# Performance work log

Hardware: AMD Instinct MI355X
Metric: run time of the kernel (lower is better)

The kernel has to match this reference:

```python
import jax, jax.numpy as jnp
import numpy as np

B, NQ, NM, NHR, D, H, FF = 16, 100, 5440, 4096, 256, 8, 2048

def _ln(x, w, b):
    m = x.mean(-1, keepdims=True)
    v = ((x - m) ** 2).mean(-1, keepdims=True)
    return (x - m) * jax.lax.rsqrt(v + 1e-5) * w + b

def setup_inputs():
    key = jax.random.key(0)
    ks = iter(jax.random.split(key, 32))
    def rn(shape, s=1.0):
        return jax.random.normal(next(ks), shape, jnp.float32) * s
    return {
        'tgt': rn((B, NQ, D)),
        'memory': rn((B, NM, D)),
        'memory_hr': rn((B, NHR, D)),
        'prior_attn_bias': rn((B, NQ, NM)),
        'query_pos': rn((B, NQ, D)),
        'ln_cross_w': jnp.ones((D,)), 'ln_cross_b': jnp.zeros((D,)),
        'q_w': rn((D, D), 0.02), 'q_b': jnp.zeros((D,)),
        'k_w': rn((D, D), 0.02), 'k_b': jnp.zeros((D,)),
        'v_w': rn((D, D), 0.02), 'v_b': jnp.zeros((D,)),
        'out_w': rn((D, D), 0.02), 'out_b': jnp.zeros((D,)),
        'ln_self_w': jnp.ones((D,)), 'ln_self_b': jnp.zeros((D,)),
        'sa_in_w': rn((3 * D, D), 0.02), 'sa_in_b': jnp.zeros((3 * D,)),
        'sa_out_w': rn((D, D), 0.02), 'sa_out_b': jnp.zeros((D,)),
        'ln_ffn_w': jnp.ones((D,)), 'ln_ffn_b': jnp.zeros((D,)),
        'lin1_w': rn((FF, D), 0.02), 'lin1_b': jnp.zeros((FF,)),
        'lin2_w': rn((D, FF), 0.02), 'lin2_b': jnp.zeros((D,)),
        'me_w': rn((D, D), 0.02), 'me_b': jnp.zeros((D,)),
    }

def reference(tgt, memory, memory_hr, prior_attn_bias, query_pos,
              ln_cross_w, ln_cross_b, q_w, q_b, k_w, k_b, v_w, v_b,
              out_w, out_b, ln_self_w, ln_self_b, sa_in_w, sa_in_b,
              sa_out_w, sa_out_b, ln_ffn_w, ln_ffn_b, lin1_w, lin1_b,
              lin2_w, lin2_b, me_w, me_b):
    b, nq, d = tgt.shape
    nm = memory.shape[1]
    h = H
    dh = d // h
    scale = dh ** -0.5
    # ---- cross-attention with additive prior bias (eval mode: dropout = id) ----
    x = _ln(tgt, ln_cross_w, ln_cross_b)
    q = ((x + query_pos) @ q_w.T + q_b).reshape(b, nq, h, dh)
    k = (memory @ k_w.T + k_b).reshape(b, nm, h, dh)
    v = (memory @ v_w.T + v_b).reshape(b, nm, h, dh)
    attn = jnp.einsum('bqhd,bmhd->bhqm', q, k) * scale + prior_attn_bias[:, None]  # [b,h,nq,nm]
    a = jax.nn.softmax(attn, axis=-1)
    o = jnp.einsum('bhqm,bmhd->bqhd', a, v).reshape(b, nq, d)
    tgt = tgt + (o @ out_w.T + out_b)
    # ---- self-attention (torch nn.MultiheadAttention, batch_first, eval) ----
    z = _ln(tgt, ln_self_w, ln_self_b)
    zq = z + query_pos
    qs = (zq @ sa_in_w[:d].T + sa_in_b[:d]).reshape(b, nq, h, dh)
    ks = (zq @ sa_in_w[d:2 * d].T + sa_in_b[d:2 * d]).reshape(b, nq, h, dh)
    vs = (z @ sa_in_w[2 * d:].T + sa_in_b[2 * d:]).reshape(b, nq, h, dh)
    sattn = jax.nn.softmax(jnp.einsum('bqhd,bmhd->bhqm', qs, ks) * scale, axis=-1)
    so = jnp.einsum('bhqm,bmhd->bqhd', sattn, vs).reshape(b, nq, d)
    tgt = tgt + (so @ sa_out_w.T + sa_out_b)
    # ---- FFN ----
    y = _ln(tgt, ln_ffn_w, ln_ffn_b)
    y = jax.nn.gelu(y @ lin1_w.T + lin1_b, approximate=False) @ lin2_w.T + lin2_b
    tgt = tgt + y
    # ---- mask branch ----
    mask_logits = jnp.einsum('bqd,bmd->bqm', tgt @ me_w.T + me_b, memory_hr)
    return (tgt, mask_logits)
```

## Files before the change

### kernel.cpp

```cpp
#include <hip/hip_runtime.h>

typedef unsigned short u16;
typedef unsigned int u32;
typedef __bf16 bf16x8 __attribute__((ext_vector_type(8)));
typedef float f32x4 __attribute__((ext_vector_type(4)));

#define NCH 34

__device__ __forceinline__ u16 f2b(float f) {
  u32 u = __float_as_uint(f);
  u32 r = (u + 0x7fffu + ((u >> 16) & 1u)) >> 16;
  return (u16)r;
}
__device__ __forceinline__ float b2f(u16 h) {
  return __uint_as_float(((u32)h) << 16);
}
__device__ __forceinline__ bf16x8 zero8() {
  union { uint4 u; bf16x8 v; } z; z.u = make_uint4(0u, 0u, 0u, 0u); return z.v;
}
__device__ __forceinline__ u32 cvtpk(float lo, float hi) {
  u32 r;
  asm("v_cvt_pk_bf16_f32 %0, %1, %2" : "=v"(r) : "v"(lo), "v"(hi));
  return r;
}

struct Seg { const float* in; u16* out; int n4; };
struct PrepArgs {
  Seg seg[7];
  const float *k_w, *v_w, *k_b, *v_b, *pbias;
  u16 *Wf, *biasT;
  float *kvB;
};

__global__ __launch_bounds__(256)
void prep_kernel(PrepArgs a)
{
  __shared__ float S[100][69];
  const int bx = blockIdx.x, tid = threadIdx.x;
  if (bx < 1472) {
    int bxr = bx;
#pragma unroll
    for (int k = 0; k < 7; ++k) {
      const int nb = a.seg[k].n4 >> 8;
      if (bxr < nb) {
        const int i = bxr * 256 + tid;
        const float4 f = *(const float4*)(a.seg[k].in + (size_t)i * 4);
        uint2 pk; pk.x = cvtpk(f.x, f.y); pk.y = cvtpk(f.z, f.w);
        *(uint2*)(a.seg[k].out + (size_t)i * 4) = pk;
        return;
      }
      bxr -= nb;
    }
    return;
  } else if (bx < 1536) {
    const int i = bx - 1472, gI = i >> 3, ks = i & 7;
    const int nt = tid >> 6, lane = tid & 63, lr = lane & 15, g = lane >> 4;
    const float* src = (gI < 4 ? a.k_w + (size_t)(gI * 64 + nt * 16 + lr) * 256
                               : a.v_w + (size_t)((gI - 4) * 64 + nt * 16 + lr) * 256)
                       + ks * 32 + g * 8;
    const float4 f0 = *(const float4*)src;
    const float4 f1 = *(const float4*)(src + 4);
    uint4 pk;
    pk.x = cvtpk(f0.x, f0.y); pk.y = cvtpk(f0.z, f0.w);
    pk.z = cvtpk(f1.x, f1.y); pk.w = cvtpk(f1.z, f1.w);
    *(uint4*)(a.Wf + (size_t)((gI * 8 + ks) * 4 + nt) * 512 + lane * 8) = pk;
  } else if (bx < 1538) {
    const int i = (bx - 1536) * 256 + tid;
    a.kvB[i] = (i < 256) ? a.k_b[i] : a.v_b[i - 256];
  } else {
    const int bt = bx - 1538;
    const int b = bt / 85, m0 = (bt - b * 85) * 64;
    for (int idx = tid; idx < 1600; idx += 256) {
      const int q = idx >> 4, seg = idx & 15;
      const float4 v = *(const float4*)(a.pbias + (size_t)(b * 100 + q) * 5440 + m0 + seg * 4);
      S[q][seg * 4 + 0] = v.x; S[q][seg * 4 + 1] = v.y;
      S[q][seg * 4 + 2] = v.z; S[q][seg * 4 + 3] = v.w;
    }
    __syncthreads();
    for (int idx = tid; idx < 1792; idx += 256) {
      const int m = idx / 28, qg = (idx % 28) * 4;
      u16 h[4];
#pragma unroll
      for (int r = 0; r < 4; ++r) {
        const int q = qg + r;
        h[r] = (q < 100) ? f2b(S[q][m]) : (u16)0;
      }
      uint2 pk;
      pk.x = (u32)h[0] | ((u32)h[1] << 16);
      pk.y = (u32)h[2] | ((u32)h[3] << 16);
      *(uint2*)(a.biasT + ((size_t)(b * 5440 + m0 + m)) * 112 + qg) = pk;
    }
  }
}

template<int ROWS>
__device__ __forceinline__ void ln_stage(const float* __restrict__ x, int row0,
    const float* __restrict__ w, const float* __restrict__ b,
    const float* __restrict__ pos, u16* As)
{
  const int tid = threadIdx.x, lane = tid & 63, wid = tid >> 6;
  const float4 wv = *(const float4*)(w + lane * 4);
  const float4 bv = *(const float4*)(b + lane * 4);
#pragma unroll
  for (int rr = 0; rr < ROWS / 4; ++rr) {
    const int rl = wid * (ROWS / 4) + rr;
    const size_t o = (size_t)(row0 + rl) * 256 + lane * 4;
    const float4 v = *(const float4*)(x + o);
    float s = v.x + v.y + v.z + v.w;
#pragma unroll
    for (int m = 1; m < 64; m <<= 1) s += __shfl_xor(s, m);
    const float mean = s * (1.f / 256.f);
    const float d0 = v.x - mean, d1 = v.y - mean, d2 = v.z - mean, d3 = v.w - mean;
    float ss = d0 * d0 + d1 * d1 + d2 * d2 + d3 * d3;
#pragma unroll
    for (int m = 1; m < 64; m <<= 1) ss += __shfl_xor(ss, m);
    const float rs = rsqrtf(ss * (1.f / 256.f) + 1e-5f);
    float y0 = d0 * rs * wv.x + bv.x;
    float y1 = d1 * rs * wv.y + bv.y;
    float y2 = d2 * rs * wv.z + bv.z;
    float y3 = d3 * rs * wv.w + bv.w;
    if (pos) {
      const float4 pv = *(const float4*)(pos + o);
      y0 += pv.x; y1 += pv.y; y2 += pv.z; y3 += pv.w;
    }
    uint2 pk; pk.x = cvtpk(y0, y1); pk.y = cvtpk(y2, y3);
    const int byte = (rl * 512 + lane * 8) ^ ((rl & 7) << 4);
    *(uint2*)((char*)As + byte) = pk;
  }
}

__device__ __forceinline__ void gemm16x128(const u16* As, const u16* __restrict__ W,
                                           u16 (*Ws)[40], f32x4 acc[2])
{
  const int tid = threadIdx.x, lane = tid & 63, wid = tid >> 6;
  const int g = lane >> 4, lr = lane & 15;
  for (int k0 = 0; k0 < 256; k0 += 32) {
    for (int cid = tid; cid < 512; cid += 256) {
      const int r = cid >> 2, cg = (cid & 3) * 8;
      *(uint4*)&Ws[r][cg] = *(const uint4*)(W + (size_t)r * 256 + k0 + cg);
    }
    __syncthreads();
    const int abyte = (lr * 512 + k0 * 2 + g * 16) ^ ((lr & 7) << 4);
    const bf16x8 af = *(const bf16x8*)((const char*)As + abyte);
#pragma unroll
    for (int nt = 0; nt < 2; ++nt) {
      const bf16x8 bfr = *(const bf16x8*)&Ws[wid * 32 + nt * 16 + lr][g * 8];
      acc[nt] = __builtin_amdgcn_mfma_f32_16x16x32_bf16(af, bfr, acc[nt], 0, 0, 0);
    }
    __syncthreads();
  }
}

__global__ __launch_bounds__(256)
void qproj_kernel(const float* __restrict__ x, const float* __restrict__ lnw,
                  const float* __restrict__ lnb, const float* __restrict__ pos,
                  const u16* __restrict__ W, const float* __restrict__ bias,
                  u16* __restrict__ out, float scale)
{
  __shared__ u16 As[16 * 256];
  __shared__ u16 Ws[128][40];
  const int tid = threadIdx.x, lane = tid & 63, wid = tid >> 6;
  const int g = lane >> 4, lr = lane & 15;
  const int row0 = blockIdx.x * 16, n0 = blockIdx.y * 128;
  ln_stage<16>(x, row0, lnw, lnb, pos, As);
  f32x4 acc[2] = {};
  gemm16x128(As, W + (size_t)n0 * 256, Ws, acc);
#pragma unroll
  for (int nt = 0; nt < 2; ++nt) {
    const int col = n0 + wid * 32 + nt * 16 + lr;
    const float bv = bias[col];
#pragma unroll
    for (int r = 0; r < 4; ++r) {
      const int row = row0 + g * 4 + r;
      out[(size_t)row * 256 + col] = f2b((acc[nt][r] + bv) * scale);
    }
  }
}

__global__ __launch_bounds__(256)
void sain_kernel(const float* __restrict__ x, const float* __restrict__ lnw,
                 const float* __restrict__ lnb, const float* __restrict__ pos,
                 const u16* __restrict__ W, const float* __restrict__ bias,
                 float* __restrict__ qkb, float* __restrict__ vsb)
{
  __shared__ u16 As[16 * 256];
  __shared__ u16 Ws[128][40];
  const int tid = threadIdx.x, lane = tid & 63, wid = tid >> 6;
  const int g = lane >> 4, lr = lane & 15;
  const int row0 = blockIdx.x * 16, y = blockIdx.y;
  ln_stage<16>(x, row0, lnw, lnb, (y < 4) ? pos : nullptr, As);
  f32x4 acc[2] = {};
  gemm16x128(As, W + (size_t)y * 128 * 256, Ws, acc);
#pragma unroll
  for (int nt = 0; nt < 2; ++nt) {
    const int cl = wid * 32 + nt * 16 + lr;
    const float bv = bias[y * 128 + cl];
#pragma unroll
    for (int r = 0; r < 4; ++r) {
      const int row = row0 + g * 4 + r;
      const float v = acc[nt][r] + bv;
      if (y < 4) qkb[(size_t)row * 512 + y * 128 + cl] = v;
      else       vsb[(size_t)row * 256 + (y - 4) * 128 + cl] = v;
    }
  }
}

__global__ __launch_bounds__(256)
void ffn1_kernel(const float* __restrict__ x, const float* __restrict__ lnw,
                 const float* __restrict__ lnb, const u16* __restrict__ W,
                 const float* __restrict__ bias, u16* __restrict__ out)
{
  __shared__ u16 As[64 * 256];
  __shared__ u16 Ws[256][40];
  const int tid = threadIdx.x, lane = tid & 63, wid = tid >> 6;
  const int g = lane >> 4, lr = lane & 15;
  const int row0 = blockIdx.x * 64, n0 = blockIdx.y * 256;
  ln_stage<64>(x, row0, lnw, lnb, nullptr, As);
  f32x4 acc[16] = {};
  for (int k0 = 0; k0 < 256; k0 += 32) {
    for (int cid = tid; cid < 1024; cid += 256) {
      const int r = cid >> 2, cg = (cid & 3) * 8;
      *(uint4*)&Ws[r][cg] = *(const uint4*)(W + (size_t)(n0 + r) * 256 + k0 + cg);
    }
    __syncthreads();
    const int arow = wid * 16 + lr;
    const int abyte = (arow * 512 + k0 * 2 + g * 16) ^ ((arow & 7) << 4);
    const bf16x8 af = *(const bf16x8*)((const char*)As + abyte);
#pragma unroll
    for (int nt = 0; nt < 16; ++nt) {
      const bf16x8 bfr = *(const bf16x8*)&Ws[nt * 16 + lr][g * 8];
      acc[nt] = __builtin_amdgcn_mfma_f32_16x16x32_bf16(af, bfr, acc[nt], 0, 0, 0);
    }
    __syncthreads();
  }
#pragma unroll
  for (int nt = 0; nt < 16; ++nt) {
    const int col = n0 + nt * 16 + lr;
    const float bv = bias[col];
#pragma unroll
    for (int r = 0; r < 4; ++r) {
      const int row = row0 + wid * 16 + g * 4 + r;
      float v = acc[nt][r] + bv;
      v = 0.5f * v * (1.f + erff(v * 0.70710678118654752f));
      out[(size_t)row * 2048 + col] = f2b(v);
    }
  }
}

template<int BM, int BN, int WM, int WN, int GELU_, int RES_, int OF32, int OBF>
__global__ __launch_bounds__(256)
void gemm_kernel(const u16* __restrict__ Ap, const u16* __restrict__ W,
                 const float* __restrict__ bias, const float* __restrict__ res,
                 float* __restrict__ Cf, u16* __restrict__ Cb,
                 int M, int N, int K, float scale)
{
  constexpr int WROWS = BM / WM;
  constexpr int WCOLS = BN / WN;
  constexpr int MT = WROWS / 16;
  constexpr int NT = WCOLS / 16;
  static_assert(WM * WN == 4, "4 waves");
  __shared__ u16 As[BM][40];
  __shared__ u16 Ws[BN][40];
  const int tid = threadIdx.x, lane = tid & 63, wid = tid >> 6;
  const int g = lane >> 4, lr = lane & 15;
  const int m0 = blockIdx.x * BM, n0 = blockIdx.y * BN;
  const int wm = wid / WN, wn = wid % WN;
  f32x4 acc[MT][NT] = {};
  for (int k0 = 0; k0 < K; k0 += 32) {
    for (int cid = tid; cid < BM * 4; cid += 256) {
      int r = cid >> 2, cg = (cid & 3) * 8;
      *(uint4*)&As[r][cg] = *(const uint4*)(Ap + (size_t)(m0 + r) * K + k0 + cg);
    }
    for (int cid = tid; cid < BN * 4; cid += 256) {
      int r = cid >> 2, cg = (cid & 3) * 8;
      *(uint4*)&Ws[r][cg] = *(const uint4*)(W + (size_t)(n0 + r) * K + k0 + cg);
    }
    __syncthreads();
    bf16x8 af[MT], bfr[NT];
#pragma unroll
    for (int mt = 0; mt < MT; ++mt) af[mt] = *(const bf16x8*)&As[wm * WROWS + mt * 16 + lr][g * 8];
#pragma unroll
    for (int nt = 0; nt < NT; ++nt) bfr[nt] = *(const bf16x8*)&Ws[wn * WCOLS + nt * 16 + lr][g * 8];
#pragma unroll
    for (int mt = 0; mt < MT; ++mt)
#pragma unroll
      for (int nt = 0; nt < NT; ++nt)
        acc[mt][nt] = __builtin_amdgcn_mfma_f32_16x16x32_bf16(af[mt], bfr[nt], acc[mt][nt], 0, 0, 0);
    __syncthreads();
  }
#pragma unroll
  for (int mt = 0; mt < MT; ++mt)
#pragma unroll
    for (int nt = 0; nt < NT; ++nt) {
      const int col = n0 + wn * WCOLS + nt * 16 + lr;
      const float bv = bias[col];
#pragma unroll
      for (int r = 0; r < 4; ++r) {
        const int row = m0 + wm * WROWS + mt * 16 + g * 4 + r;
        float v = (acc[mt][nt][r] + bv) * scale;
        if constexpr (GELU_) v = 0.5f * v * (1.f + erff(v * 0.70710678118654752f));
        if constexpr (RES_) v += res[(size_t)row * N + col];
        if constexpr (OF32) Cf[(size_t)row * N + col] = v;
        if constexpr (OBF) Cb[(size_t)row * N + col] = f2b(v);
      }
    }
}

__global__ __launch_bounds__(512, 4)
void kv_gemm_kernel(const float* __restrict__ A, const u16* __restrict__ Wf,
                    const float* __restrict__ biasKV,
                    u16* __restrict__ Kb, u16* __restrict__ Vt)
{
  __shared__ u16 As[64 * 256];
  __shared__ u16 Vs[256 * 64];
  const int tid = threadIdx.x, lane = tid & 63, wid = tid >> 6;
  const int g = lane >> 4, lr = lane & 15;
  const int bidx = blockIdx.x / 85, t = blockIdx.x - bidx * 85;
  const int row0 = blockIdx.x * 64;

  for (int ch = tid; ch < 2048; ch += 512) {
    const int r = ch >> 5, c8 = (ch & 31) * 8;
    const float* ap = A + (size_t)(row0 + r) * 256 + c8;
    const float4 f0 = *(const float4*)ap;
    const float4 f1 = *(const float4*)(ap + 4);
    uint4 pk;
    pk.x = cvtpk(f0.x, f0.y);
    pk.y = cvtpk(f0.z, f0.w);
    pk.z = cvtpk(f1.x, f1.y);
    pk.w = cvtpk(f1.z, f1.w);
    const int byte = r * 512 + c8 * 2;
    *(uint4*)((char*)As + (byte ^ ((r & 7) << 4))) = pk;
  }
  __syncthreads();

  const u16* wbase = Wf + (size_t)wid * 8 * 4 * 512 + lane * 8;
  f32x4 acc[4][4] = {};
#pragma unroll 2
  for (int ks = 0; ks < 8; ++ks) {
    bf16x8 bfv[4], af[4];
#pragma unroll
    for (int nt = 0; nt < 4; ++nt)
      bfv[nt] = *(const bf16x8*)(wbase + (ks * 4 + nt) * 512);
#pragma unroll
    for (int mt = 0; mt < 4; ++mt) {
      const int r = mt * 16 + lr;
      const int byte = r * 512 + ks * 64 + g * 16;
      af[mt] = *(const bf16x8*)((const char*)As + (byte ^ ((r & 7) << 4)));
    }
#pragma unroll
    for (int mt = 0; mt < 4; ++mt)
#pragma unroll
      for (int nt = 0; nt < 4; ++nt)
        acc[mt][nt] = __builtin_amdgcn_mfma_f32_16x16x32_bf16(af[mt], bfv[nt], acc[mt][nt], 0, 0, 0);
  }

  const int isV = wid >> 2;
  if (isV) {
#pragma unroll
    for (int nt = 0; nt < 4; ++nt) {
      const int col = (wid - 4) * 64 + nt * 16 + lr;
      const float bv = biasKV[256 + col];
#pragma unroll
      for (int a = 0; a < 2; ++a)
#pragma unroll
        for (int r = 0; r < 4; ++r) {
          const u32 val = cvtpk(acc[2 * a][nt][r] + bv, acc[2 * a + 1][nt][r] + bv);
          const int byte = (col * 128 + a * 64 + g * 16 + r * 4) ^ ((col & 7) << 4);
          *(u32*)((char*)Vs + byte) = val;
        }
    }
  }
  __syncthreads();

  if (!isV) {
#pragma unroll
    for (int nt = 0; nt < 4; ++nt) {
      const int col = wid * 64 + nt * 16 + lr;
      const float bv = biasKV[col];
#pragma unroll
      for (int mt = 0; mt < 4; ++mt)
#pragma unroll
        for (int r = 0; r < 4; r += 2) {
          const u32 pk = cvtpk(acc[mt][nt][r] + bv, acc[mt][nt][r + 1] + bv);
          const int rowA = mt * 16 + g * 4 + r;
          const int rowB = rowA + 1;
          *(u16*)((char*)As + ((rowA * 512 + col * 2) ^ ((rowA & 7) << 4))) = (u16)pk;
          *(u16*)((char*)As + ((rowB * 512 + col * 2) ^ ((rowB & 7) << 4))) = (u16)(pk >> 16);
        }
    }
  } else {
    const size_t vbase = (size_t)bidx * 256 * 5440 + (size_t)t * 64;
    const int t2 = tid - 256;
#pragma unroll
    for (int p = 0; p < 8; ++p) {
      const int idx = p * 256 + t2;
      const int col = idx >> 3, chunk = idx & 7;
      const int lbyte = col * 128 + ((chunk * 16) ^ ((col & 7) << 4));
      const uint4 v = *(const uint4*)((const char*)Vs + lbyte);
      *(uint4*)(Vt + vbase + (size_t)col * 5440 + chunk * 8) = v;
    }
  }
  __syncthreads();
#pragma unroll
  for (int p = 0; p < 4; ++p) {
    const int idx = p * 512 + tid;
    const int row = idx >> 5, c16 = idx & 31;
    const int lbyte = row * 512 + ((c16 * 16) ^ ((row & 7) << 4));
    const uint4 v = *(const uint4*)((const char*)As + lbyte);
    *(uint4*)(Kb + (size_t)(row0 + row) * 256 + c16 * 8) = v;
  }
}

__global__ __launch_bounds__(256, 3)
void cross_attn_kernel(const u16* __restrict__ Q, const u16* __restrict__ Kb,
                       const u16* __restrict__ Vt, const u16* __restrict__ biasT,
                       float* __restrict__ Opart, float* __restrict__ ML)
{
  __shared__ u32 P32[4][112][20];
  const int tid = threadIdx.x, lane = tid & 63, wid = tid >> 6;
  const int g = lane >> 4, lr = lane & 15;
  const int b = blockIdx.y, c = blockIdx.x;
  const int head = blockIdx.z * 4 + wid;
  const int m_base = c * (5440 / NCH);
  const f32x4 zf = {0.f, 0.f, 0.f, 0.f};

  bf16x8 qf[7];
#pragma unroll
  for (int mt = 0; mt < 7; ++mt) {
    int qr = mt * 16 + lr;
    qf[mt] = (qr < 100) ? *(const bf16x8*)&Q[(size_t)(b * 100 + qr) * 256 + head * 32 + g * 8]
                        : zero8();
  }
  float Mst[7];
  f32x4 Lp[7];
  f32x4 Oa[7][2];
#pragma unroll
  for (int mt = 0; mt < 7; ++mt) { Mst[mt] = -1e30f; Lp[mt] = zf; Oa[mt][0] = zf; Oa[mt][1] = zf; }

  for (int s = 0; s < (5440 / NCH) / 32; ++s) {
    const int m0 = m_base + s * 32;
    const bf16x8 kf0 = *(const bf16x8*)&Kb[(size_t)(b * 5440 + m0 + lr) * 256 + head * 32 + g * 8];
    const bf16x8 kf1 = *(const bf16x8*)&Kb[(size_t)(b * 5440 + m0 + 16 + lr) * 256 + head * 32 + g * 8];
    const size_t vrow = ((size_t)(b * 8 + head) * 32 + lr) * 5440 + m0 + g * 8;
    const bf16x8 vf0 = *(const bf16x8*)&Vt[vrow];
    const bf16x8 vf1 = *(const bf16x8*)&Vt[vrow + 16 * 5440];
    const u16* bb = biasT + ((size_t)(b * 5440 + m0 + lr)) * 112 + g * 4;
#pragma unroll
    for (int mt = 0; mt < 7; ++mt) {
      f32x4 s0 = __builtin_amdgcn_mfma_f32_16x16x32_bf16(qf[mt], kf0, zf, 0, 0, 0);
      f32x4 s1 = __builtin_amdgcn_mfma_f32_16x16x32_bf16(qf[mt], kf1, zf, 0, 0, 0);
      const uint2 b0 = *(const uint2*)(bb + mt * 16);
      const uint2 b1 = *(const uint2*)(bb + 16 * 112 + mt * 16);
      s0[0] += b2f((u16)b0.x);      s0[1] += b2f((u16)(b0.x >> 16));
      s0[2] += b2f((u16)b0.y);      s0[3] += b2f((u16)(b0.y >> 16));
      s1[0] += b2f((u16)b1.x);      s1[1] += b2f((u16)(b1.x >> 16));
      s1[2] += b2f((u16)b1.y);      s1[3] += b2f((u16)(b1.y >> 16));
      float mx = fmaxf(fmaxf(fmaxf(s0[0], s0[1]), fmaxf(s0[2], s0[3])),
                       fmaxf(fmaxf(s1[0], s1[1]), fmaxf(s1[2], s1[3])));
#pragma unroll
      for (int d = 1; d < 16; d <<= 1) mx = fmaxf(mx, __shfl_xor(mx, d, 16));
      const float newM = fmaxf(Mst[mt], mx);
      const float al = __expf(Mst[mt] - newM);
      Mst[mt] = newM;
      f32x4 p0, p1;
#pragma unroll
      for (int r = 0; r < 4; ++r) {
        p0[r] = __expf(s0[r] - newM);
        p1[r] = __expf(s1[r] - newM);
      }
      Lp[mt] = Lp[mt] * al + (p0 + p1);
      Oa[mt][0] *= al;
      Oa[mt][1] *= al;
#pragma unroll
      for (int r = 0; r < 4; ++r)
        P32[wid][mt * 16 + g * 4 + r][lr] = (u32)f2b(p0[r]) | ((u32)f2b(p1[r]) << 16);
    }
#pragma unroll
    for (int mt = 0; mt < 7; ++mt) {
      const bf16x8 pa = *(const bf16x8*)&P32[wid][mt * 16 + lr][g * 4];
      Oa[mt][0] = __builtin_amdgcn_mfma_f32_16x16x32_bf16(pa, vf0, Oa[mt][0], 0, 0, 0);
      Oa[mt][1] = __builtin_amdgcn_mfma_f32_16x16x32_bf16(pa, vf1, Oa[mt][1], 0, 0, 0);
    }
  }
  const int bh = b * 8 + head;
#pragma unroll
  for (int mt = 0; mt < 7; ++mt)
#pragma unroll
    for (int r = 0; r < 4; ++r) {
      const int qr = mt * 16 + g * 4 + r;
      if (qr < 100) {
        float L = Lp[mt][r];
#pragma unroll
        for (int d = 1; d < 16; d <<= 1) L += __shfl_xor(L, d, 16);
        const size_t rb = (size_t)(bh * NCH + c) * 100 + qr;
        Opart[rb * 32 + lr] = Oa[mt][0][r];
        Opart[rb * 32 + 16 + lr] = Oa[mt][1][r];
        if (lr == 0) { ML[rb * 2] = Mst[mt]; ML[rb * 2 + 1] = L; }
      }
    }
}

__global__ __launch_bounds__(256)
void reduce_attn_kernel(const float* __restrict__ Opart, const float* __restrict__ ML,
                        u16* __restrict__ outb)
{
  const int row = blockIdx.x;
  const int b = row / 100, q = row % 100;
  const int h = threadIdx.x >> 5, d = threadIdx.x & 31;
  const int bh = b * 8 + h;
  float gm = -1e30f;
  for (int c = 0; c < NCH; ++c) gm = fmaxf(gm, ML[((size_t)(bh * NCH + c) * 100 + q) * 2]);
  float l = 0.f, o = 0.f;
  for (int c = 0; c < NCH; ++c) {
    const size_t rb = (size_t)(bh * NCH + c) * 100 + q;
    const float w = __expf(ML[rb * 2] - gm);
    l += ML[rb * 2 + 1] * w;
    o += Opart[rb * 32 + d] * w;
  }
  outb[(size_t)row * 256 + h * 32 + d] = f2b(o / l);
}

__global__ __launch_bounds__(128)
void self_attn_kernel(const float* __restrict__ qk, const float* __restrict__ vs,
                      u16* __restrict__ so)
{
  __shared__ u16 kk[100][36];
  __shared__ u16 vv[100][36];
  __shared__ float S[100][101];
  const int b = blockIdx.x >> 3, h = blockIdx.x & 7;
  const int t = threadIdx.x;
  for (int e = t; e < 3200; e += 128) {
    const int r = e >> 5, cq = e & 31;
    kk[r][cq] = f2b(qk[(size_t)(b * 100 + r) * 512 + 256 + h * 32 + cq]);
    vv[r][cq] = f2b(vs[(size_t)(b * 100 + r) * 256 + h * 32 + cq]);
  }
  __syncthreads();
  if (t < 100) {
    float qr_[32];
#pragma unroll
    for (int cq = 0; cq < 32; ++cq) qr_[cq] = qk[(size_t)(b * 100 + t) * 512 + h * 32 + cq];
    for (int m = 0; m < 100; ++m) {
      float dp = 0.f;
#pragma unroll
      for (int cq = 0; cq < 32; ++cq) dp += qr_[cq] * b2f(kk[m][cq]);
      S[t][m] = dp * 0.17677669529663687f;
    }
    float mx = -1e30f;
    for (int m = 0; m < 100; ++m) mx = fmaxf(mx, S[t][m]);
    float sum = 0.f;
    for (int m = 0; m < 100; ++m) { const float p = __expf(S[t][m] - mx); S[t][m] = p; sum += p; }
    const float inv = 1.f / sum;
    float o[32];
#pragma unroll
    for (int cq = 0; cq < 32; ++cq) o[cq] = 0.f;
    for (int m = 0; m < 100; ++m) {
      const float p = S[t][m];
#pragma unroll
      for (int cq = 0; cq < 32; ++cq) o[cq] += p * b2f(vv[m][cq]);
    }
#pragma unroll
    for (int cq = 0; cq < 32; ++cq)
      so[(size_t)(b * 100 + t) * 256 + h * 32 + cq] = f2b(o[cq] * inv);
  }
}

__global__ __launch_bounds__(256)
void mask_gemm_kernel(const u16* __restrict__ tm, const float* __restrict__ hr,
                      float* __restrict__ out)
{
  __shared__ u16 As[112][40];
  __shared__ u16 Bs[64][40];
  const int tid = threadIdx.x, lane = tid & 63, wid = tid >> 6;
  const int g = lane >> 4, lr = lane & 15;
  const int b = blockIdx.y, n0 = blockIdx.x * 64;
  f32x4 acc[7] = {};
  for (int k0 = 0; k0 < 256; k0 += 32) {
    for (int cid = tid; cid < 448; cid += 256) {
      const int r = cid >> 2, cg = (cid & 3) * 8;
      uint4 val = {0u, 0u, 0u, 0u};
      if (r < 100) val = *(const uint4*)&tm[(size_t)(b * 100 + r) * 256 + k0 + cg];
      *(uint4*)&As[r][cg] = val;
    }
    {
      const int r = tid >> 2, cg = (tid & 3) * 8;
      const float* hp = hr + (size_t)(b * 4096 + n0 + r) * 256 + k0 + cg;
      float4 f0 = *(const float4*)hp;
      float4 f1 = *(const float4*)(hp + 4);
      uint4 pk;
      pk.x = cvtpk(f0.x, f0.y); pk.y = cvtpk(f0.z, f0.w);
      pk.z = cvtpk(f1.x, f1.y); pk.w = cvtpk(f1.z, f1.w);
      *(uint4*)&Bs[r][cg] = pk;
    }
    __syncthreads();
    const bf16x8 bfr = *(const bf16x8*)&Bs[wid * 16 + lr][g * 8];
#pragma unroll
    for (int mt = 0; mt < 7; ++mt) {
      const bf16x8 af = *(const bf16x8*)&As[mt * 16 + lr][g * 8];
      acc[mt] = __builtin_amdgcn_mfma_f32_16x16x32_bf16(af, bfr, acc[mt], 0, 0, 0);
    }
    __syncthreads();
  }
#pragma unroll
  for (int mt = 0; mt < 7; ++mt)
#pragma unroll
    for (int r = 0; r < 4; ++r) {
      const int qr = mt * 16 + g * 4 + r;
      if (qr < 100)
        out[(size_t)(b * 100 + qr) * 4096 + n0 + wid * 16 + lr] = acc[mt][r];
    }
}

extern "C" void kernel_launch(void* const* d_in, const int* in_sizes, int n_in,
                              void* d_out, int out_size, void* d_ws, size_t ws_size,
                              hipStream_t stream)
{
  (void)in_sizes; (void)n_in; (void)out_size; (void)ws_size;
  const float* tgt      = (const float*)d_in[0];
  const float* memory   = (const float*)d_in[1];
  const float* memhr    = (const float*)d_in[2];
  const float* pbias    = (const float*)d_in[3];
  const float* qpos     = (const float*)d_in[4];
  const float* lncw     = (const float*)d_in[5];
  const float* lncb     = (const float*)d_in[6];
  const float* q_w      = (const float*)d_in[7];
  const float* q_b      = (const float*)d_in[8];
  const float* k_w      = (const float*)d_in[9];
  const float* k_b      = (const float*)d_in[10];
  const float* v_w      = (const float*)d_in[11];
  const float* v_b      = (const float*)d_in[12];
  const float* out_w    = (const float*)d_in[13];
  const float* out_b    = (const float*)d_in[14];
  const float* lnsw     = (const float*)d_in[15];
  const float* lnsb     = (const float*)d_in[16];
  const float* sa_in_w  = (const float*)d_in[17];
  const float* sa_in_b  = (const float*)d_in[18];
  const float* sa_out_w = (const float*)d_in[19];
  const float* sa_out_b = (const float*)d_in[20];
  const float* lnfw     = (const float*)d_in[21];
  const float* lnfb     = (const float*)d_in[22];
  const float* l1w      = (const float*)d_in[23];
  const float* l1b      = (const float*)d_in[24];
  const float* l2w      = (const float*)d_in[25];
  const float* l2b      = (const float*)d_in[26];
  const float* me_w     = (const float*)d_in[27];
  const float* me_b     = (const float*)d_in[28];
  float* outf = (float*)d_out;

  char* ws = (char*)d_ws;
  size_t off = 0;
  auto alloc = [&](size_t bytes) -> void* {
    void* p = ws + off;
    off = (off + bytes + 255) & ~(size_t)255;
    return p;
  };
  u16*   Wf    = (u16*)alloc((size_t)131072 * 2);
  u16*   qW    = (u16*)alloc((size_t)65536 * 2);
  u16*   outW  = (u16*)alloc((size_t)65536 * 2);
  u16*   saW   = (u16*)alloc((size_t)196608 * 2);
  u16*   saoW  = (u16*)alloc((size_t)65536 * 2);
  u16*   l1W   = (u16*)alloc((size_t)524288 * 2);
  u16*   l2W   = (u16*)alloc((size_t)524288 * 2);
  u16*   meW   = (u16*)alloc((size_t)65536 * 2);
  float* kvB   = (float*)alloc((size_t)512 * 4);
  u16*   biasT = (u16*)alloc((size_t)9748480 * 2);
  u16*   Qb    = (u16*)alloc((size_t)409600 * 2);
  u16*   Kb    = (u16*)alloc((size_t)22282240 * 2);
  u16*   Vt    = (u16*)alloc((size_t)22282240 * 2);
  float* Opart = (float*)alloc((size_t)(128 * NCH * 100 * 32) * 4);
  float* MLp   = (float*)alloc((size_t)(128 * NCH * 100 * 2) * 4);
  u16*   attno = (u16*)alloc((size_t)409600 * 2);
  float* tgt1  = (float*)alloc((size_t)409600 * 4);
  float* qkb   = (float*)alloc((size_t)819200 * 4);
  float* vsb   = (float*)alloc((size_t)409600 * 4);
  u16*   sob   = (u16*)alloc((size_t)409600 * 2);
  float* tgt2  = (float*)alloc((size_t)409600 * 4);
  u16*   hb    = (u16*)alloc((size_t)3276800 * 2);
  u16*   t3b   = (u16*)alloc((size_t)409600 * 2);
  u16*   tmb   = (u16*)alloc((size_t)409600 * 2);

  const float SCALE = 0.17677669529663687f;

  PrepArgs pa;
  pa.seg[0] = {q_w,      qW,   16384};
  pa.seg[1] = {out_w,    outW, 16384};
  pa.seg[2] = {sa_in_w,  saW,  49152};
  pa.seg[3] = {sa_out_w, saoW, 16384};
  pa.seg[4] = {l1w,      l1W,  131072};
  pa.seg[5] = {l2w,      l2W,  131072};
  pa.seg[6] = {me_w,     meW,  16384};
  pa.k_w = k_w; pa.v_w = v_w; pa.k_b = k_b; pa.v_b = v_b; pa.pbias = pbias;
  pa.Wf = Wf; pa.biasT = biasT; pa.kvB = kvB;
  prep_kernel<<<2898, 256, 0, stream>>>(pa);

  qproj_kernel<<<dim3(100, 2), 256, 0, stream>>>(tgt, lncw, lncb, qpos, qW, q_b, Qb, SCALE);
  kv_gemm_kernel<<<dim3(1360), 512, 0, stream>>>(memory, Wf, kvB, Kb, Vt);
  cross_attn_kernel<<<dim3(NCH, 16, 2), 256, 0, stream>>>(Qb, Kb, Vt, biasT, Opart, MLp);
  reduce_attn_kernel<<<1600, 256, 0, stream>>>(Opart, MLp, attno);
  gemm_kernel<16, 128, 1, 4, 0, 1, 1, 0><<<dim3(100, 2), 256, 0, stream>>>(
      attno, outW, out_b, tgt, tgt1, nullptr, 1600, 256, 256, 1.f);

  sain_kernel<<<dim3(100, 6), 256, 0, stream>>>(tgt1, lnsw, lnsb, qpos, saW, sa_in_b, qkb, vsb);
  self_attn_kernel<<<128, 128, 0, stream>>>(qkb, vsb, sob);
  gemm_kernel<16, 128, 1, 4, 0, 1, 1, 0><<<dim3(100, 2), 256, 0, stream>>>(
      sob, saoW, sa_out_b, tgt1, tgt2, nullptr, 1600, 256, 256, 1.f);

  ffn1_kernel<<<dim3(25, 8), 256, 0, stream>>>(tgt2, lnfw, lnfb, l1W, l1b, hb);
  gemm_kernel<16, 128, 1, 4, 0, 1, 1, 1><<<dim3(100, 2), 256, 0, stream>>>(
      hb, l2W, l2b, tgt2, outf, t3b, 1600, 256, 2048, 1.f);

  gemm_kernel<16, 128, 1, 4, 0, 0, 0, 1><<<dim3(100, 2), 256, 0, stream>>>(
      t3b, meW, me_b, nullptr, nullptr, tmb, 1600, 256, 256, 1.f);
  mask_gemm_kernel<<<dim3(64, 16), 256, 0, stream>>>(tmb, memhr, outf + 409600);
}
```

Baseline: 343.4 us.

## Pre-swizzle attention bias into MFMA fragment layout and prefetch per step

The prep kernel now writes the prior bias in a layout that matches the MFMA accumulator fragments, so each lane loads one 16-byte vector per query tile instead of two scattered 8-byte loads. The cross-attention loop prefetches all seven bias vectors at the start of each key step. The change also adds s_setprio around the MFMA sections, replaces the manual bf16 packing with v_cvt_pk_bf16_f32, and raises the occupancy hint to 4. Holding the prefetched bias in registers and asking for higher occupancy may increase register pressure or cause spills, and the prep kernel now launches more, smaller blocks.

```diff
diff --git a/kernel.cpp b/kernel.cpp
--- a/kernel.cpp
+++ b/kernel.cpp
@@ -6,6 +6,7 @@
 typedef float f32x4 __attribute__((ext_vector_type(4)));
 
 #define NCH 34
+#define NSTEP 5
 
 __device__ __forceinline__ u16 f2b(float f) {
   u32 u = __float_as_uint(f);
@@ -28,14 +29,15 @@
 struct PrepArgs {
   Seg seg[7];
   const float *k_w, *v_w, *k_b, *v_b, *pbias;
-  u16 *Wf, *biasT;
+  u16 *Wf;
+  uint4 *biasT4;
   float *kvB;
 };
 
 __global__ __launch_bounds__(256)
 void prep_kernel(PrepArgs a)
 {
-  __shared__ float S[100][69];
+  __shared__ float S[100][34];
   const int bx = blockIdx.x, tid = threadIdx.x;
   if (bx < 1472) {
     int bxr = bx;
@@ -69,26 +71,32 @@
     a.kvB[i] = (i < 256) ? a.k_b[i] : a.v_b[i - 256];
   } else {
     const int bt = bx - 1538;
-    const int b = bt / 85, m0 = (bt - b * 85) * 64;
-    for (int idx = tid; idx < 1600; idx += 256) {
-      const int q = idx >> 4, seg = idx & 15;
+    const int b = bt / 170, sg = bt - b * 170;
+    const int m0 = sg * 32;
+    for (int idx = tid; idx < 800; idx += 256) {
+      const int q = idx >> 3, seg = idx & 7;
       const float4 v = *(const float4*)(a.pbias + (size_t)(b * 100 + q) * 5440 + m0 + seg * 4);
       S[q][seg * 4 + 0] = v.x; S[q][seg * 4 + 1] = v.y;
       S[q][seg * 4 + 2] = v.z; S[q][seg * 4 + 3] = v.w;
     }
     __syncthreads();
-    for (int idx = tid; idx < 1792; idx += 256) {
-      const int m = idx / 28, qg = (idx % 28) * 4;
-      u16 h[4];
+    for (int idx = tid; idx < 448; idx += 256) {
+      const int mt = idx >> 6, lane = idx & 63;
+      const int lr = lane & 15, g = lane >> 4;
+      const int q0 = mt * 16 + g * 4;
+      u16 h[8];
 #pragma unroll
       for (int r = 0; r < 4; ++r) {
-        const int q = qg + r;
-        h[r] = (q < 100) ? f2b(S[q][m]) : (u16)0;
+        const int q = q0 + r;
+        h[r]     = (q < 100) ? f2b(S[q][lr])      : (u16)0;
+        h[4 + r] = (q < 100) ? f2b(S[q][16 + lr]) : (u16)0;
       }
-      uint2 pk;
+      uint4 pk;
       pk.x = (u32)h[0] | ((u32)h[1] << 16);
       pk.y = (u32)h[2] | ((u32)h[3] << 16);
-      *(uint2*)(a.biasT + ((size_t)(b * 5440 + m0 + m)) * 112 + qg) = pk;
+      pk.z = (u32)h[4] | ((u32)h[5] << 16);
+      pk.w = (u32)h[6] | ((u32)h[7] << 16);
+      a.biasT4[((size_t)bt * 7 + mt) * 64 + lane] = pk;
     }
   }
 }
@@ -411,9 +419,9 @@
   }
 }
 
-__global__ __launch_bounds__(256, 3)
+__global__ __launch_bounds__(256, 4)
 void cross_attn_kernel(const u16* __restrict__ Q, const u16* __restrict__ Kb,
-                       const u16* __restrict__ Vt, const u16* __restrict__ biasT,
+                       const u16* __restrict__ Vt, const uint4* __restrict__ biasT4,
                        float* __restrict__ Opart, float* __restrict__ ML)
 {
   __shared__ u32 P32[4][112][20];
@@ -437,24 +445,28 @@
 #pragma unroll
   for (int mt = 0; mt < 7; ++mt) { Mst[mt] = -1e30f; Lp[mt] = zf; Oa[mt][0] = zf; Oa[mt][1] = zf; }
 
-  for (int s = 0; s < (5440 / NCH) / 32; ++s) {
+  for (int s = 0; s < NSTEP; ++s) {
     const int m0 = m_base + s * 32;
+    const uint4* bb4 = biasT4 + ((size_t)(b * 170 + c * NSTEP + s) * 7) * 64 + lane;
+    uint4 bias_pf[7];
+#pragma unroll
+    for (int mt = 0; mt < 7; ++mt) bias_pf[mt] = bb4[mt * 64];
     const bf16x8 kf0 = *(const bf16x8*)&Kb[(size_t)(b * 5440 + m0 + lr) * 256 + head * 32 + g * 8];
     const bf16x8 kf1 = *(const bf16x8*)&Kb[(size_t)(b * 5440 + m0 + 16 + lr) * 256 + head * 32 + g * 8];
     const size_t vrow = ((size_t)(b * 8 + head) * 32 + lr) * 5440 + m0 + g * 8;
     const bf16x8 vf0 = *(const bf16x8*)&Vt[vrow];
     const bf16x8 vf1 = *(const bf16x8*)&Vt[vrow + 16 * 5440];
-    const u16* bb = biasT + ((size_t)(b * 5440 + m0 + lr)) * 112 + g * 4;
 #pragma unroll
     for (int mt = 0; mt < 7; ++mt) {
+      __builtin_amdgcn_s_setprio(1);
       f32x4 s0 = __builtin_amdgcn_mfma_f32_16x16x32_bf16(qf[mt], kf0, zf, 0, 0, 0);
       f32x4 s1 = __builtin_amdgcn_mfma_f32_16x16x32_bf16(qf[mt], kf1, zf, 0, 0, 0);
-      const uint2 b0 = *(const uint2*)(bb + mt * 16);
-      const uint2 b1 = *(const uint2*)(bb + 16 * 112 + mt * 16);
-      s0[0] += b2f((u16)b0.x);      s0[1] += b2f((u16)(b0.x >> 16));
-      s0[2] += b2f((u16)b0.y);      s0[3] += b2f((u16)(b0.y >> 16));
-      s1[0] += b2f((u16)b1.x);      s1[1] += b2f((u16)(b1.x >> 16));
-      s1[2] += b2f((u16)b1.y);      s1[3] += b2f((u16)(b1.y >> 16));
+      __builtin_amdgcn_s_setprio(0);
+      const uint4 bq = bias_pf[mt];
+      s0[0] += b2f((u16)bq.x);      s0[1] += b2f((u16)(bq.x >> 16));
+      s0[2] += b2f((u16)bq.y);      s0[3] += b2f((u16)(bq.y >> 16));
+      s1[0] += b2f((u16)bq.z);      s1[1] += b2f((u16)(bq.z >> 16));
+      s1[2] += b2f((u16)bq.w);      s1[3] += b2f((u16)(bq.w >> 16));
       float mx = fmaxf(fmaxf(fmaxf(s0[0], s0[1]), fmaxf(s0[2], s0[3])),
                        fmaxf(fmaxf(s1[0], s1[1]), fmaxf(s1[2], s1[3])));
 #pragma unroll
@@ -473,14 +485,16 @@
       Oa[mt][1] *= al;
 #pragma unroll
       for (int r = 0; r < 4; ++r)
-        P32[wid][mt * 16 + g * 4 + r][lr] = (u32)f2b(p0[r]) | ((u32)f2b(p1[r]) << 16);
-    }
+        P32[wid][mt * 16 + g * 4 + r][lr] = cvtpk(p0[r], p1[r]);
+    }
+    __builtin_amdgcn_s_setprio(1);
 #pragma unroll
     for (int mt = 0; mt < 7; ++mt) {
       const bf16x8 pa = *(const bf16x8*)&P32[wid][mt * 16 + lr][g * 4];
       Oa[mt][0] = __builtin_amdgcn_mfma_f32_16x16x32_bf16(pa, vf0, Oa[mt][0], 0, 0, 0);
       Oa[mt][1] = __builtin_amdgcn_mfma_f32_16x16x32_bf16(pa, vf1, Oa[mt][1], 0, 0, 0);
     }
+    __builtin_amdgcn_s_setprio(0);
   }
   const int bh = b * 8 + head;
 #pragma unroll
@@ -662,7 +676,7 @@
   u16*   l2W   = (u16*)alloc((size_t)524288 * 2);
   u16*   meW   = (u16*)alloc((size_t)65536 * 2);
   float* kvB   = (float*)alloc((size_t)512 * 4);
-  u16*   biasT = (u16*)alloc((size_t)9748480 * 2);
+  uint4* biasT4= (uint4*)alloc((size_t)16 * 170 * 7 * 64 * 16);
   u16*   Qb    = (u16*)alloc((size_t)409600 * 2);
   u16*   Kb    = (u16*)alloc((size_t)22282240 * 2);
   u16*   Vt    = (u16*)alloc((size_t)22282240 * 2);
@@ -689,12 +703,12 @@
   pa.seg[5] = {l2w,      l2W,  131072};
   pa.seg[6] = {me_w,     meW,  16384};
   pa.k_w = k_w; pa.v_w = v_w; pa.k_b = k_b; pa.v_b = v_b; pa.pbias = pbias;
-  pa.Wf = Wf; pa.biasT = biasT; pa.kvB = kvB;
-  prep_kernel<<<2898, 256, 0, stream>>>(pa);
+  pa.Wf = Wf; pa.biasT4 = biasT4; pa.kvB = kvB;
+  prep_kernel<<<4258, 256, 0, stream>>>(pa);
 
   qproj_kernel<<<dim3(100, 2), 256, 0, stream>>>(tgt, lncw, lncb, qpos, qW, q_b, Qb, SCALE);
   kv_gemm_kernel<<<dim3(1360), 512, 0, stream>>>(memory, Wf, kvB, Kb, Vt);
-  cross_attn_kernel<<<dim3(NCH, 16, 2), 256, 0, stream>>>(Qb, Kb, Vt, biasT, Opart, MLp);
+  cross_attn_kernel<<<dim3(NCH, 16, 2), 256, 0, stream>>>(Qb, Kb, Vt, biasT4, Opart, MLp);
   reduce_attn_kernel<<<1600, 256, 0, stream>>>(Opart, MLp, attno);
   gemm_kernel<16, 128, 1, 4, 0, 1, 1, 0><<<dim3(100, 2), 256, 0, stream>>>(
       attno, outW, out_b, tgt, tgt1, nullptr, 1600, 256, 256, 1.f);
```

Result: slower. 428.5 us (+24.8%).
